# Kernel tuning notes

Hardware: AMD Instinct MI355X
Metric: run time of the kernel (lower is better)

Reference implementation:

```python
import jax, jax.numpy as jnp
import numpy as np

HIDDEN = 512
HEADS = 8
NORM = 1.0 / np.sqrt(HIDDEN // HEADS)  # torch: 1/sqrt(tensor(dim_k)//head) = 1/8


def setup_inputs() -> dict:
    key = jax.random.key(0)
    ks = jax.random.split(key, 14)
    B, N, D = 2, 2048, HIDDEN
    s = 0.02
    d = {
        "x_re": jax.random.normal(ks[0], (B, N, D), dtype=jnp.float32),
        "x_im": jax.random.normal(ks[1], (B, N, D), dtype=jnp.float32),
    }
    names = ["Wq_re", "Wq_im", "bq_re", "bq_im",
             "Wk_re", "Wk_im", "bk_re", "bk_im",
             "Wv_re", "Wv_im", "bv_re", "bv_im"]
    for i, nm in enumerate(names):
        shape = (D, D) if nm.startswith("W") else (D,)
        d[nm] = jax.random.normal(ks[2 + i], shape, dtype=jnp.float32) * s
    return d


def reference(x_re, x_im,
              Wq_re, Wq_im, bq_re, bq_im,
              Wk_re, Wk_im, bk_re, bk_im,
              Wv_re, Wv_im, bv_re, bv_im):
    B, N, D = x_re.shape
    h, dk = HEADS, D // HEADS
    x = jax.lax.complex(x_re, x_im)
    Wq = jax.lax.complex(Wq_re, Wq_im); bq = jax.lax.complex(bq_re, bq_im)
    Wk = jax.lax.complex(Wk_re, Wk_im); bk = jax.lax.complex(bk_re, bk_im)
    Wv = jax.lax.complex(Wv_re, Wv_im); bv = jax.lax.complex(bv_re, bv_im)

    def proj(W, b):  # torch nn.Linear: x @ W.T + b, then split heads -> [B,h,N,dk]
        y = x @ W.T + b
        return y.reshape(B, N, h, dk).transpose(0, 2, 1, 3)

    q, k, v = proj(Wq, bq), proj(Wk, bk), proj(Wv, bv)
    # complex matmul (no conjugation, matching torch.matmul), scaled
    dist = jnp.einsum("bhnd,bhmd->bhnm", q, k) * NORM
    probs = jax.nn.softmax(jnp.abs(dist), axis=-1).astype(jnp.complex64)
    att = jnp.einsum("bhnm,bhmd->bhnd", probs, v)
    att = att.transpose(0, 2, 1, 3).reshape(B, N, D)
    # real-view output [B, N, D, 2]
    return jnp.stack([att.real, att.imag], axis=-1)
```

## Files before the change

### kernel.cpp

```cpp
#include <hip/hip_runtime.h>
#include <hip/hip_bf16.h>
#include <math.h>

#define B_ 2
#define N_ 2048
#define D_ 512
#define H_ 8
#define DK_ 64
#define M_ (B_ * N_)

typedef short s16x8 __attribute__((ext_vector_type(8)));
typedef short s16x4 __attribute__((ext_vector_type(4)));
typedef float fx4   __attribute__((ext_vector_type(4)));
typedef int   ix4   __attribute__((ext_vector_type(4)));

static __device__ __forceinline__ short f2bf(float f) {
    __hip_bfloat16 h = __float2bfloat16(f);
    return __builtin_bit_cast(short, h);
}
static __device__ __forceinline__ float bf2f(short s) {
    unsigned int u = ((unsigned int)(unsigned short)s) << 16;
    return __builtin_bit_cast(float, u);
}
static __device__ __forceinline__ float fexp2(float x) {
#if __has_builtin(__builtin_amdgcn_exp2f)
    return __builtin_amdgcn_exp2f(x);
#else
    return exp2f(x);
#endif
}
static __device__ __forceinline__ float fsqrt_(float x) {
#if __has_builtin(__builtin_amdgcn_sqrtf)
    return __builtin_amdgcn_sqrtf(x);
#else
    return sqrtf(x);
#endif
}
static __device__ __forceinline__ int pack_tr(float a, float b) {
    unsigned ua = __builtin_bit_cast(unsigned, a);
    unsigned ub = __builtin_bit_cast(unsigned, b);
    return (int)((ua >> 16) | (ub & 0xFFFF0000u));
}

#define MFMA16(a, b, c) __builtin_amdgcn_mfma_f32_16x16x32_bf16(a, b, c, 0, 0, 0)

#define C2_ 0.18033688f
#define M0_ 16.0f

__global__ __launch_bounds__(256, 2)
void qkproj_mfma(const float* __restrict__ xr, const float* __restrict__ xi,
                 const float* __restrict__ W0r, const float* __restrict__ W0i,
                 const float* __restrict__ b0r, const float* __restrict__ b0i,
                 const float* __restrict__ W1r, const float* __restrict__ W1i,
                 const float* __restrict__ b1r, const float* __restrict__ b1i,
                 short* __restrict__ o0r, short* __restrict__ o0i,
                 short* __restrict__ o1r, short* __restrict__ o1i)
{
    __shared__ short sA[2][128][40];
    __shared__ short sB[2][64][40];

    const int tid = threadIdx.x;
    const int w = tid >> 6, l = tid & 63, lg = l >> 4, lc = l & 15;
    const int wr = w >> 1, wc = w & 1;
    const int bn = blockIdx.x, bm = blockIdx.y, z = blockIdx.z;
    const float* Wr = z ? W1r : W0r;
    const float* Wi = z ? W1i : W0i;
    const float* br = z ? b1r : b0r;
    const float* bi = z ? b1i : b0i;
    short* outr = z ? o1r : o0r;
    short* outi = z ? o1i : o0i;

    const int srow = tid >> 3, scol = (tid & 7) * 4;
    int aoff = (bm * 128 + srow) * D_ + scol;
    int boff = (bn * 64 + srow) * D_ + scol;

    float4 rA[8], rB[4];
    auto issue = [&]() {
#pragma unroll
        for (int u = 0; u < 8; ++u) {
            const float* src = (u >= 4) ? xi : xr;
            rA[u] = *(const float4*)&src[aoff + (u & 3) * 32 * D_];
        }
#pragma unroll
        for (int u = 0; u < 4; ++u) {
            const float* src = (u >= 2) ? Wi : Wr;
            rB[u] = *(const float4*)&src[boff + (u & 1) * 32 * D_];
        }
        aoff += 32; boff += 32;
    };

    fx4 Cre[4][2], Cim[4][2];
#pragma unroll
    for (int mf = 0; mf < 4; ++mf)
#pragma unroll
        for (int nf = 0; nf < 2; ++nf)
#pragma unroll
            for (int j = 0; j < 4; ++j) { Cre[mf][nf][j] = 0.f; Cim[mf][nf][j] = 0.f; }

    issue();
    for (int k0 = 0; k0 < D_; k0 += 32) {
        __syncthreads();
#pragma unroll
        for (int u = 0; u < 8; ++u) {
            int comp = u >> 2, row = (u & 3) * 32 + srow;
            float vv[4] = {rA[u].x, rA[u].y, rA[u].z, rA[u].w};
            s16x4 hv;
#pragma unroll
            for (int q = 0; q < 4; ++q) hv[q] = f2bf(vv[q]);
            *(s16x4*)&sA[comp][row][scol] = hv;
        }
#pragma unroll
        for (int u = 0; u < 4; ++u) {
            int comp = u >> 1, row = (u & 1) * 32 + srow;
            float vv[4] = {rB[u].x, rB[u].y, rB[u].z, rB[u].w};
            s16x4 hv;
#pragma unroll
            for (int q = 0; q < 4; ++q) hv[q] = f2bf(vv[q]);
            *(s16x4*)&sB[comp][row][scol] = hv;
        }
        __syncthreads();
        if (k0 + 32 < D_) issue();

        s16x8 a[2][4];
#pragma unroll
        for (int comp = 0; comp < 2; ++comp)
#pragma unroll
            for (int mf = 0; mf < 4; ++mf)
                a[comp][mf] = *(const s16x8*)&sA[comp][wr * 64 + mf * 16 + lc][lg * 8];
        s16x8 bfr[2][2], bin[2];
#pragma unroll
        for (int comp = 0; comp < 2; ++comp)
#pragma unroll
            for (int nf = 0; nf < 2; ++nf)
                bfr[comp][nf] = *(const s16x8*)&sB[comp][wc * 32 + nf * 16 + lc][lg * 8];
#pragma unroll
        for (int nf = 0; nf < 2; ++nf) bin[nf] = bfr[1][nf] ^ (short)0x8000;

        __builtin_amdgcn_s_setprio(1);
#pragma unroll
        for (int mf = 0; mf < 4; ++mf)
#pragma unroll
            for (int nf = 0; nf < 2; ++nf) {
                Cre[mf][nf] = MFMA16(a[0][mf], bfr[0][nf], Cre[mf][nf]);
                Cre[mf][nf] = MFMA16(a[1][mf], bin[nf],    Cre[mf][nf]);
                Cim[mf][nf] = MFMA16(a[0][mf], bfr[1][nf], Cim[mf][nf]);
                Cim[mf][nf] = MFMA16(a[1][mf], bfr[0][nf], Cim[mf][nf]);
            }
        __builtin_amdgcn_s_setprio(0);
    }

    const int bb = (bm * 128) >> 11;
#pragma unroll
    for (int nf = 0; nf < 2; ++nf) {
        const int c = bn * 64 + wc * 32 + nf * 16 + lc;
        const float brv = br[c], biv = bi[c];
        const int h = c >> 6, dd = c & 63;
        const int n00 = (bm * 128 + wr * 64 + lg * 4) & (N_ - 1);
        size_t obase = (((size_t)(bb * H_ + h) * N_) + n00) * DK_ + dd;
#pragma unroll
        for (int mf = 0; mf < 4; ++mf)
#pragma unroll
            for (int j = 0; j < 4; ++j) {
                size_t o = obase + (size_t)(mf * 16 + j) * DK_;
                outr[o] = f2bf(Cre[mf][nf][j] + brv);
                outi[o] = f2bf(Cim[mf][nf][j] + biv);
            }
    }
}

__global__ __launch_bounds__(256, 2)
void vproj_mfma(const float* __restrict__ xr, const float* __restrict__ xi,
                const float* __restrict__ Wr, const float* __restrict__ Wi,
                const float* __restrict__ br, const float* __restrict__ bi,
                short* __restrict__ outr, short* __restrict__ outi)
{
    __shared__ short sA[2][2][64][40];
    __shared__ short sB[2][2][64][40];

    const int tid = threadIdx.x;
    const int w = tid >> 6, l = tid & 63, lg = l >> 4, lc = l & 15;
    const int wr = w >> 1, wc = w & 1;
    const int bn = blockIdx.x, bm = blockIdx.y;

    const int srow = tid >> 3, scol = (tid & 7) * 4;
    int aoff = (bm * 64 + srow) * D_ + scol;
    int boff = (bn * 64 + srow) * D_ + scol;

    float4 rA[4], rB[4];
    auto issue = [&]() {
#pragma unroll
        for (int u = 0; u < 4; ++u) {
            const float* src = (u >= 2) ? xi : xr;
            rA[u] = *(const float4*)&src[aoff + (u & 1) * 32 * D_];
        }
#pragma unroll
        for (int u = 0; u < 4; ++u) {
            const float* src = (u >= 2) ? Wi : Wr;
            rB[u] = *(const float4*)&src[boff + (u & 1) * 32 * D_];
        }
        aoff += 32; boff += 32;
    };

    fx4 Cre[2][2], Cim[2][2];
#pragma unroll
    for (int mf = 0; mf < 2; ++mf)
#pragma unroll
        for (int nf = 0; nf < 2; ++nf)
#pragma unroll
            for (int j = 0; j < 4; ++j) { Cre[mf][nf][j] = 0.f; Cim[mf][nf][j] = 0.f; }

    issue();
    for (int k0 = 0; k0 < D_; k0 += 32) {
        __syncthreads();
#pragma unroll
        for (int u = 0; u < 4; ++u) {
            int comp = u >> 1, row = (u & 1) * 32 + srow;
            float vv[4] = {rA[u].x, rA[u].y, rA[u].z, rA[u].w};
            s16x4 hv, lv;
#pragma unroll
            for (int q = 0; q < 4; ++q) {
                short hh = f2bf(vv[q]);
                hv[q] = hh;
                lv[q] = f2bf(vv[q] - bf2f(hh));
            }
            *(s16x4*)&sA[comp][0][row][scol] = hv;
            *(s16x4*)&sA[comp][1][row][scol] = lv;
        }
#pragma unroll
        for (int u = 0; u < 4; ++u) {
            int comp = u >> 1, row = (u & 1) * 32 + srow;
            float vv[4] = {rB[u].x, rB[u].y, rB[u].z, rB[u].w};
            s16x4 hv, lv;
#pragma unroll
            for (int q = 0; q < 4; ++q) {
                short hh = f2bf(vv[q]);
                hv[q] = hh;
                lv[q] = f2bf(vv[q] - bf2f(hh));
            }
            *(s16x4*)&sB[comp][0][row][scol] = hv;
            *(s16x4*)&sB[comp][1][row][scol] = lv;
        }
        __syncthreads();
        if (k0 + 32 < D_) issue();

        s16x8 a[2][2][2];
#pragma unroll
        for (int comp = 0; comp < 2; ++comp)
#pragma unroll
            for (int s = 0; s < 2; ++s)
#pragma unroll
                for (int mf = 0; mf < 2; ++mf)
                    a[comp][s][mf] = *(const s16x8*)&sA[comp][s][wr * 32 + mf * 16 + lc][lg * 8];
        s16x8 bfr[2][2][2], bin[2][2];
#pragma unroll
        for (int comp = 0; comp < 2; ++comp)
#pragma unroll
            for (int s = 0; s < 2; ++s)
#pragma unroll
                for (int nf = 0; nf < 2; ++nf)
                    bfr[comp][s][nf] = *(const s16x8*)&sB[comp][s][wc * 32 + nf * 16 + lc][lg * 8];
#pragma unroll
        for (int s = 0; s < 2; ++s)
#pragma unroll
            for (int nf = 0; nf < 2; ++nf)
                bin[s][nf] = bfr[1][s][nf] ^ (short)0x8000;

        __builtin_amdgcn_s_setprio(1);
#pragma unroll
        for (int mf = 0; mf < 2; ++mf)
#pragma unroll
            for (int nf = 0; nf < 2; ++nf) {
                fx4 cr = Cre[mf][nf], ci = Cim[mf][nf];
                cr = MFMA16(a[0][0][mf], bfr[0][0][nf], cr);
                cr = MFMA16(a[1][0][mf], bin[0][nf],    cr);
                ci = MFMA16(a[0][0][mf], bfr[1][0][nf], ci);
                ci = MFMA16(a[1][0][mf], bfr[0][0][nf], ci);
                cr = MFMA16(a[0][0][mf], bfr[0][1][nf], cr);
                cr = MFMA16(a[0][1][mf], bfr[0][0][nf], cr);
                cr = MFMA16(a[1][0][mf], bin[1][nf],    cr);
                cr = MFMA16(a[1][1][mf], bin[0][nf],    cr);
                ci = MFMA16(a[0][0][mf], bfr[1][1][nf], ci);
                ci = MFMA16(a[0][1][mf], bfr[1][0][nf], ci);
                ci = MFMA16(a[1][0][mf], bfr[0][1][nf], ci);
                ci = MFMA16(a[1][1][mf], bfr[0][0][nf], ci);
                Cre[mf][nf] = cr; Cim[mf][nf] = ci;
            }
        __builtin_amdgcn_s_setprio(0);
    }

    const int bb = (bm * 64) >> 11;
#pragma unroll
    for (int nf = 0; nf < 2; ++nf) {
        const int c = bn * 64 + wc * 32 + nf * 16 + lc;
        const float brv = br[c], biv = bi[c];
        const int h = c >> 6, dd = c & 63;
#pragma unroll
        for (int mf = 0; mf < 2; ++mf) {
            int m0 = bm * 64 + wr * 32 + mf * 16 + lg * 4;
            int n0 = m0 & (N_ - 1);
            s16x4 pr, pi;
#pragma unroll
            for (int j = 0; j < 4; ++j) {
                pr[j] = f2bf(Cre[mf][nf][j] + brv);
                pi[j] = f2bf(Cim[mf][nf][j] + biv);
            }
            size_t o = (((size_t)(bb * H_ + h) * DK_) + dd) * N_ + n0;
            *(s16x4*)&outr[o] = pr;
            *(s16x4*)&outi[o] = pi;
        }
    }
}

#define NT_ (N_ / 64)
#define NR_ (NT_ / 2)

static __device__ __forceinline__ int swz8(int row, int slot) {
    return (slot + (row & 7) + 2 * ((row >> 3) & 3)) & 7;
}

__global__ __launch_bounds__(512, 2)
void attn_mfma(const short* __restrict__ qr, const short* __restrict__ qi,
               const short* __restrict__ kr, const short* __restrict__ ki,
               const short* __restrict__ vtr, const short* __restrict__ vti,
               float* __restrict__ out)
{
    __shared__ short sK [2][2][2][64][64];
    __shared__ short sVt[2][2][2][64][64];

    const int tid = threadIdx.x;
    const int w = tid >> 6, l = tid & 63, lg = l >> 4, lc = l & 15;
    const int kg = w & 1, qw = w >> 1;

    const int dlin = blockIdx.y * 16 + blockIdx.x;
    const int xcd = dlin & 7, slot = dlin >> 3;
    const int bh = xcd * 2 + (slot >> 4);
    const int qt = slot & 15;
    const int b = bh >> 3, h = bh & 7;

    s16x8 Qr[2][2], Qi_[2][2], Qin[2][2];
#pragma unroll
    for (int qh = 0; qh < 2; ++qh) {
        size_t base = ((size_t)bh * N_ + (size_t)qt * 128 + qw * 32 + qh * 16 + lc) * DK_ + lg * 8;
#pragma unroll
        for (int c = 0; c < 2; ++c) {
            Qr[qh][c]  = *(const s16x8*)&qr[base + c * 32];
            Qi_[qh][c] = *(const s16x8*)&qi[base + c * 32];
            Qin[qh][c] = Qi_[qh][c] ^ (short)0x8000;
        }
    }

    s16x8 onesf;
#pragma unroll
    for (int u = 0; u < 8; ++u) onesf[u] = (short)0x3F80;

    fx4 o_re[2][4], o_im[2][4], o_l[2];
#pragma unroll
    for (int qh = 0; qh < 2; ++qh) {
#pragma unroll
        for (int dt = 0; dt < 4; ++dt)
#pragma unroll
            for (int j = 0; j < 4; ++j) { o_re[qh][dt][j] = 0.f; o_im[qh][dt][j] = 0.f; }
#pragma unroll
        for (int j = 0; j < 4; ++j) o_l[qh][j] = 0.f;
    }

    const int rS = ((lc >> 2) << 3) | (lc & 3);
    const int bqs = lg + (lc & 3) + 2 * (lc >> 2);
    const int bvs = lg + (lc & 7) + 2 * (lc >> 3);

    const int srow = tid >> 3, cs = tid & 7;
    const int sw = swz8(srow, cs) * 8;
    int koff = bh * (N_ * DK_) + srow * DK_ + cs * 8;
    int voff = bh * (DK_ * N_) + srow * N_ + cs * 8;

    s16x8 rgK[2][2], rgV[2][2];
    auto issue = [&]() {
#pragma unroll
        for (int g = 0; g < 2; ++g) {
            rgK[g][0] = *(const s16x8*)&kr [koff + g * 64 * DK_];
            rgK[g][1] = *(const s16x8*)&ki [koff + g * 64 * DK_];
            rgV[g][0] = *(const s16x8*)&vtr[voff + g * 64];
            rgV[g][1] = *(const s16x8*)&vti[voff + g * 64];
        }
        koff += 128 * DK_; voff += 128;
    };
    auto stage = [&](int nb) {
#pragma unroll
        for (int g = 0; g < 2; ++g)
#pragma unroll
            for (int comp = 0; comp < 2; ++comp) {
                *(s16x8*)&sK [nb][g][comp][srow][sw] = rgK[g][comp];
                *(s16x8*)&sVt[nb][g][comp][srow][sw] = rgV[g][comp];
            }
    };

    issue();
    stage(0);
    for (int r = 0; r < NR_; ++r) {
        const int cb = r & 1;
        __syncthreads();
        if (r + 1 < NR_) issue();

        fx4 are[2][4], aim[2][4];
#pragma unroll
        for (int qh = 0; qh < 2; ++qh)
#pragma unroll
            for (int t = 0; t < 4; ++t)
#pragma unroll
                for (int j = 0; j < 4; ++j) { are[qh][t][j] = 0.f; aim[qh][t][j] = 0.f; }

        __builtin_amdgcn_s_setprio(1);
#pragma unroll
        for (int t = 0; t < 4; ++t) {
            const int row = rS + ((t & 1) << 2) + ((t >> 1) << 5);
#pragma unroll
            for (int c = 0; c < 2; ++c) {
                const int sl = ((bqs + 4 * ((c + t) & 1)) & 7) * 8;
                s16x8 Krf = *(const s16x8*)&sK[cb][kg][0][row][sl];
                s16x8 Kif = *(const s16x8*)&sK[cb][kg][1][row][sl];
#pragma unroll
                for (int qh = 0; qh < 2; ++qh) {
                    are[qh][t] = MFMA16(Krf, Qr[qh][c],  are[qh][t]);
                    are[qh][t] = MFMA16(Kif, Qin[qh][c], are[qh][t]);
                    aim[qh][t] = MFMA16(Kif, Qr[qh][c],  aim[qh][t]);
                    aim[qh][t] = MFMA16(Krf, Qi_[qh][c], aim[qh][t]);
                }
            }
        }
        __builtin_amdgcn_s_setprio(0);

        s16x8 Pf[2][2];
#pragma unroll
        for (int qh = 0; qh < 2; ++qh) {
            ix4 w0, w1;
#pragma unroll
            for (int t = 0; t < 4; ++t) {
                float p[4];
#pragma unroll
                for (int j = 0; j < 4; ++j) {
                    float u2 = fmaf(are[qh][t][j], are[qh][t][j], aim[qh][t][j] * aim[qh][t][j]);
                    p[j] = fexp2(fmaf(C2_, fsqrt_(u2), -M0_));
                }
                int d0 = pack_tr(p[0], p[1]);
                int d1 = pack_tr(p[2], p[3]);
                if (t == 0)      { w0[0] = d0; w0[1] = d1; }
                else if (t == 1) { w0[2] = d0; w0[3] = d1; }
                else if (t == 2) { w1[0] = d0; w1[1] = d1; }
                else             { w1[2] = d0; w1[3] = d1; }
            }
            Pf[qh][0] = __builtin_bit_cast(s16x8, w0);
            Pf[qh][1] = __builtin_bit_cast(s16x8, w1);
        }

        __builtin_amdgcn_s_setprio(1);
#pragma unroll
        for (int qh = 0; qh < 2; ++qh) {
            o_l[qh] = MFMA16(Pf[qh][0], onesf, o_l[qh]);
            o_l[qh] = MFMA16(Pf[qh][1], onesf, o_l[qh]);
        }
#pragma unroll
        for (int dt = 0; dt < 4; ++dt) {
            const int d = dt * 16 + lc;
            const int s0 = ((bvs + 4 * dt) & 7) * 8;
            const int s1 = ((bvs + 4 * dt + 4) & 7) * 8;
            s16x8 Vr0 = *(const s16x8*)&sVt[cb][kg][0][d][s0];
            s16x8 Vi0 = *(const s16x8*)&sVt[cb][kg][1][d][s0];
            s16x8 Vr1 = *(const s16x8*)&sVt[cb][kg][0][d][s1];
            s16x8 Vi1 = *(const s16x8*)&sVt[cb][kg][1][d][s1];
#pragma unroll
            for (int qh = 0; qh < 2; ++qh) {
                o_re[qh][dt] = MFMA16(Pf[qh][0], Vr0, o_re[qh][dt]);
                o_im[qh][dt] = MFMA16(Pf[qh][0], Vi0, o_im[qh][dt]);
                o_re[qh][dt] = MFMA16(Pf[qh][1], Vr1, o_re[qh][dt]);
                o_im[qh][dt] = MFMA16(Pf[qh][1], Vi1, o_im[qh][dt]);
            }
        }
        __builtin_amdgcn_s_setprio(0);

        if (r + 1 < NR_) stage(cb ^ 1);
    }

    float* red = (float*)&sK[0][0][0][0][0];
    float2* po = (float2*)out;
#pragma unroll
    for (int qh = 0; qh < 2; ++qh) {
        __syncthreads();
        if (kg == 1) {
            const int base = (qw * 64 + l) * 37;
#pragma unroll
            for (int dt = 0; dt < 4; ++dt)
#pragma unroll
                for (int j = 0; j < 4; ++j) {
                    red[base + dt * 8 + j * 2 + 0] = o_re[qh][dt][j];
                    red[base + dt * 8 + j * 2 + 1] = o_im[qh][dt][j];
                }
#pragma unroll
            for (int j = 0; j < 4; ++j) red[base + 32 + j] = o_l[qh][j];
        }
        __syncthreads();
        if (kg == 0) {
            const int base = (qw * 64 + l) * 37;
            float inv[4];
#pragma unroll
            for (int j = 0; j < 4; ++j)
                inv[j] = 1.f / (o_l[qh][j] + red[base + 32 + j]);
#pragma unroll
            for (int dt = 0; dt < 4; ++dt)
#pragma unroll
                for (int j = 0; j < 4; ++j) {
                    float re = o_re[qh][dt][j] + red[base + dt * 8 + j * 2 + 0];
                    float im = o_im[qh][dt][j] + red[base + dt * 8 + j * 2 + 1];
                    int n  = qt * 128 + qw * 32 + qh * 16 + lg * 4 + j;
                    int dg = h * 64 + dt * 16 + lc;
                    po[((size_t)b * N_ + n) * D_ + dg] =
                        make_float2(re * inv[j], im * inv[j]);
                }
        }
    }
}

extern "C" void kernel_launch(void* const* d_in, const int* in_sizes, int n_in,
                              void* d_out, int out_size, void* d_ws, size_t ws_size,
                              hipStream_t stream)
{
    const float* xr = (const float*)d_in[0];
    const float* xi = (const float*)d_in[1];
    const float* Wq_r = (const float*)d_in[2];
    const float* Wq_i = (const float*)d_in[3];
    const float* bq_r = (const float*)d_in[4];
    const float* bq_i = (const float*)d_in[5];
    const float* Wk_r = (const float*)d_in[6];
    const float* Wk_i = (const float*)d_in[7];
    const float* bk_r = (const float*)d_in[8];
    const float* bk_i = (const float*)d_in[9];
    const float* Wv_r = (const float*)d_in[10];
    const float* Wv_i = (const float*)d_in[11];
    const float* bv_r = (const float*)d_in[12];
    const float* bv_i = (const float*)d_in[13];

    short* ws = (short*)d_ws;
    const size_t SZ = (size_t)B_ * H_ * N_ * DK_;
    short* qr_  = ws + 0 * SZ;
    short* qi_  = ws + 1 * SZ;
    short* kr_  = ws + 2 * SZ;
    short* ki_  = ws + 3 * SZ;
    short* vtr_ = ws + 4 * SZ;
    short* vti_ = ws + 5 * SZ;

    dim3 qkgrid(D_ / 64, M_ / 128, 2);
    qkproj_mfma<<<qkgrid, 256, 0, stream>>>(xr, xi,
                                            Wq_r, Wq_i, bq_r, bq_i,
                                            Wk_r, Wk_i, bk_r, bk_i,
                                            qr_, qi_, kr_, ki_);
    dim3 vgrid(D_ / 64, M_ / 64);
    vproj_mfma<<<vgrid, 256, 0, stream>>>(xr, xi, Wv_r, Wv_i, bv_r, bv_i, vtr_, vti_);

    dim3 agrid(16, 16);
    attn_mfma<<<agrid, 512, 0, stream>>>(qr_, qi_, kr_, ki_, vtr_, vti_, (float*)d_out);
}
```

Baseline: 120.7 us.

## Double-buffer projection LDS tiles; read V fragments directly from global in attention

```diff
diff --git a/kernel.cpp b/kernel.cpp
--- a/kernel.cpp
+++ b/kernel.cpp
@@ -46,6 +46,8 @@
 
 #define C2_ 0.18033688f
 #define M0_ 16.0f
+
+#define QKNS_ (D_ / 32)
 
 __global__ __launch_bounds__(256, 2)
 void qkproj_mfma(const float* __restrict__ xr, const float* __restrict__ xi,
@@ -56,8 +58,8 @@
                  short* __restrict__ o0r, short* __restrict__ o0i,
                  short* __restrict__ o1r, short* __restrict__ o1i)
 {
-    __shared__ short sA[2][128][40];
-    __shared__ short sB[2][64][40];
+    __shared__ short sA[2][2][128][40];
+    __shared__ short sB[2][2][64][40];
 
     const int tid = threadIdx.x;
     const int w = tid >> 6, l = tid & 63, lg = l >> 4, lc = l & 15;
@@ -88,18 +90,7 @@
         }
         aoff += 32; boff += 32;
     };
-
-    fx4 Cre[4][2], Cim[4][2];
-#pragma unroll
-    for (int mf = 0; mf < 4; ++mf)
-#pragma unroll
-        for (int nf = 0; nf < 2; ++nf)
-#pragma unroll
-            for (int j = 0; j < 4; ++j) { Cre[mf][nf][j] = 0.f; Cim[mf][nf][j] = 0.f; }
-
-    issue();
-    for (int k0 = 0; k0 < D_; k0 += 32) {
-        __syncthreads();
+    auto stage = [&](int nb) {
 #pragma unroll
         for (int u = 0; u < 8; ++u) {
             int comp = u >> 2, row = (u & 3) * 32 + srow;
@@ -107,7 +98,7 @@
             s16x4 hv;
 #pragma unroll
             for (int q = 0; q < 4; ++q) hv[q] = f2bf(vv[q]);
-            *(s16x4*)&sA[comp][row][scol] = hv;
+            *(s16x4*)&sA[nb][comp][row][scol] = hv;
         }
 #pragma unroll
         for (int u = 0; u < 4; ++u) {
@@ -116,23 +107,37 @@
             s16x4 hv;
 #pragma unroll
             for (int q = 0; q < 4; ++q) hv[q] = f2bf(vv[q]);
-            *(s16x4*)&sB[comp][row][scol] = hv;
-        }
+            *(s16x4*)&sB[nb][comp][row][scol] = hv;
+        }
+    };
+
+    fx4 Cre[4][2], Cim[4][2];
+#pragma unroll
+    for (int mf = 0; mf < 4; ++mf)
+#pragma unroll
+        for (int nf = 0; nf < 2; ++nf)
+#pragma unroll
+            for (int j = 0; j < 4; ++j) { Cre[mf][nf][j] = 0.f; Cim[mf][nf][j] = 0.f; }
+
+    issue();
+    stage(0);
+    for (int ks = 0; ks < QKNS_; ++ks) {
+        const int cb = ks & 1;
         __syncthreads();
-        if (k0 + 32 < D_) issue();
+        if (ks + 1 < QKNS_) issue();
 
         s16x8 a[2][4];
 #pragma unroll
         for (int comp = 0; comp < 2; ++comp)
 #pragma unroll
             for (int mf = 0; mf < 4; ++mf)
-                a[comp][mf] = *(const s16x8*)&sA[comp][wr * 64 + mf * 16 + lc][lg * 8];
+                a[comp][mf] = *(const s16x8*)&sA[cb][comp][wr * 64 + mf * 16 + lc][lg * 8];
         s16x8 bfr[2][2], bin[2];
 #pragma unroll
         for (int comp = 0; comp < 2; ++comp)
 #pragma unroll
             for (int nf = 0; nf < 2; ++nf)
-                bfr[comp][nf] = *(const s16x8*)&sB[comp][wc * 32 + nf * 16 + lc][lg * 8];
+                bfr[comp][nf] = *(const s16x8*)&sB[cb][comp][wc * 32 + nf * 16 + lc][lg * 8];
 #pragma unroll
         for (int nf = 0; nf < 2; ++nf) bin[nf] = bfr[1][nf] ^ (short)0x8000;
 
@@ -147,6 +152,8 @@
                 Cim[mf][nf] = MFMA16(a[1][mf], bfr[0][nf], Cim[mf][nf]);
             }
         __builtin_amdgcn_s_setprio(0);
+
+        if (ks + 1 < QKNS_) stage(cb ^ 1);
     }
 
     const int bb = (bm * 128) >> 11;
@@ -324,8 +331,7 @@
                const short* __restrict__ vtr, const short* __restrict__ vti,
                float* __restrict__ out)
 {
-    __shared__ short sK [2][2][2][64][64];
-    __shared__ short sVt[2][2][2][64][64];
+    __shared__ short sK[2][2][2][64][64];
 
     const int tid = threadIdx.x;
     const int w = tid >> 6, l = tid & 63, lg = l >> 4, lc = l & 15;
@@ -366,33 +372,29 @@
 
     const int rS = ((lc >> 2) << 3) | (lc & 3);
     const int bqs = lg + (lc & 3) + 2 * (lc >> 2);
-    const int bvs = lg + (lc & 7) + 2 * (lc >> 3);
 
     const int srow = tid >> 3, cs = tid & 7;
     const int sw = swz8(srow, cs) * 8;
     int koff = bh * (N_ * DK_) + srow * DK_ + cs * 8;
-    int voff = bh * (DK_ * N_) + srow * N_ + cs * 8;
-
-    s16x8 rgK[2][2], rgV[2][2];
+
+    s16x8 rgK[2][2];
     auto issue = [&]() {
 #pragma unroll
         for (int g = 0; g < 2; ++g) {
-            rgK[g][0] = *(const s16x8*)&kr [koff + g * 64 * DK_];
-            rgK[g][1] = *(const s16x8*)&ki [koff + g * 64 * DK_];
-            rgV[g][0] = *(const s16x8*)&vtr[voff + g * 64];
-            rgV[g][1] = *(const s16x8*)&vti[voff + g * 64];
-        }
-        koff += 128 * DK_; voff += 128;
+            rgK[g][0] = *(const s16x8*)&kr[koff + g * 64 * DK_];
+            rgK[g][1] = *(const s16x8*)&ki[koff + g * 64 * DK_];
+        }
+        koff += 128 * DK_;
     };
     auto stage = [&](int nb) {
 #pragma unroll
         for (int g = 0; g < 2; ++g)
 #pragma unroll
-            for (int comp = 0; comp < 2; ++comp) {
-                *(s16x8*)&sK [nb][g][comp][srow][sw] = rgK[g][comp];
-                *(s16x8*)&sVt[nb][g][comp][srow][sw] = rgV[g][comp];
-            }
+            for (int comp = 0; comp < 2; ++comp)
+                *(s16x8*)&sK[nb][g][comp][srow][sw] = rgK[g][comp];
     };
+
+    const size_t vrow0 = (size_t)bh * (DK_ * N_) + (size_t)kg * 64 + lg * 8;
 
     issue();
     stage(0);
@@ -452,6 +454,7 @@
             Pf[qh][1] = __builtin_bit_cast(s16x8, w1);
         }
 
+        const size_t vb0 = vrow0 + (size_t)r * 128;
         __builtin_amdgcn_s_setprio(1);
 #pragma unroll
         for (int qh = 0; qh < 2; ++qh) {
@@ -460,13 +463,11 @@
         }
 #pragma unroll
         for (int dt = 0; dt < 4; ++dt) {
-            const int d = dt * 16 + lc;
-            const int s0 = ((bvs + 4 * dt) & 7) * 8;
-            const int s1 = ((bvs + 4 * dt + 4) & 7) * 8;
-            s16x8 Vr0 = *(const s16x8*)&sVt[cb][kg][0][d][s0];
-            s16x8 Vi0 = *(const s16x8*)&sVt[cb][kg][1][d][s0];
-            s16x8 Vr1 = *(const s16x8*)&sVt[cb][kg][0][d][s1];
-            s16x8 Vi1 = *(const s16x8*)&sVt[cb][kg][1][d][s1];
+            const size_t ro = vb0 + (size_t)(dt * 16 + lc) * N_;
+            s16x8 Vr0 = *(const s16x8*)&vtr[ro];
+            s16x8 Vi0 = *(const s16x8*)&vti[ro];
+            s16x8 Vr1 = *(const s16x8*)&vtr[ro + 32];
+            s16x8 Vi1 = *(const s16x8*)&vti[ro + 32];
 #pragma unroll
             for (int qh = 0; qh < 2; ++qh) {
                 o_re[qh][dt] = MFMA16(Pf[qh][0], Vr0, o_re[qh][dt]);
```

New measurement: 163.7 us. 35.7% more time.
